# Kernel tuning notes

Hardware: AMD Instinct MI355X
Metric: run time of the kernel (lower is better)

## Reference

```python
import jax, jax.numpy as jnp
import numpy as np

BATCH = 2      # batch_size (number of videos)
NUM_HEADS = 8


def setup_inputs() -> dict:
    key = jax.random.key(0)
    k1, k2, k3 = jax.random.split(key, 3)
    B, H, W, C = 16, 64, 64, 512
    return {
        "hidden_states": jax.random.normal(k1, (B, H, W, C), dtype=jnp.float32),
        "w_qkv": jax.random.normal(k2, (3 * C, C), dtype=jnp.float32) * (C ** -0.5),
        "b_qkv": jax.random.normal(k3, (3 * C,), dtype=jnp.float32) * 0.02,
    }


def reference(hidden_states, w_qkv, b_qkv):
    B, H, W, C = hidden_states.shape
    bs, nh = BATCH, NUM_HEADS
    f = B // bs                      # video_length
    hd = C // nh                     # head_dim
    scale = hd ** -0.5

    # qkv projection (torch Linear: x @ W.T + b)
    qkv = hidden_states @ w_qkv.T + b_qkv                       # [B,H,W,3C]
    qkv = qkv.reshape(B, H * W, 3, nh, hd)
    qkv = qkv.transpose(2, 0, 3, 1, 4).reshape(3, B * nh, H * W, hd)
    q, k, v = qkv[0], qkv[1], qkv[2]                            # [B*nh, HW, hd]

    # NOTE: original rearrange labels '(b n f)' but memory layout is (b f) n;
    # it is a pure reshape, so replicate as flat reshape (faithful to math).
    q = q.reshape(bs, nh, f, H, W, hd)
    k = k.reshape(bs, nh, f, H, W, hd)
    v = v.reshape(bs, nh, f, H, W, hd)

    # q cat is identity; k/v: prepend last frame == cyclic roll by +1 on frames
    k = jnp.roll(k, 1, axis=2)
    v = jnp.roll(v, 1, axis=2)

    q = q.reshape(bs, nh, f, H * W, hd)
    # faithful flat reshape (scrambles (h,w,c) -> (hd, HW) order, as in torch)
    k = k.reshape(bs, nh, f, hd, H * W)
    v = v.reshape(bs, nh, f, H * W, hd)

    # einsums with NO contracted index: elementwise-transpose products
    attn = jnp.einsum('bnfhw,bnfwh->bnhfw', q * scale, k)       # [bs,nh,HW,f,hd]
    attn = jax.nn.softmax(attn, axis=-1)
    x = jnp.einsum('bnhfw,bnfhw->bnhfw', attn, v)               # [bs,nh,HW,f,hd]

    # faithful flat reshape (torch .view on contiguous tensor)
    x = x.reshape(bs, nh, f, H, W, hd)
    # rearrange 'b n f h w c -> (b f) h w (n c)'
    x = x.transpose(0, 2, 3, 4, 1, 5).reshape(bs * f, H, W, nh * hd)
    return x
```

## Files before the change

### kernel.cpp

```cpp
#include <hip/hip_runtime.h>
#include <math.h>


typedef _Float16 half8 __attribute__((ext_vector_type(8)));
typedef _Float16 half4 __attribute__((ext_vector_type(4)));
typedef __fp16 fp16x2 __attribute__((ext_vector_type(2)));
typedef float f32x4 __attribute__((ext_vector_type(4)));

__device__ __forceinline__ half8 pk8(const float4 x, const float4 y) {
    fp16x2 a = __builtin_amdgcn_cvt_pkrtz(x.x, x.y);
    fp16x2 b = __builtin_amdgcn_cvt_pkrtz(x.z, x.w);
    fp16x2 c = __builtin_amdgcn_cvt_pkrtz(y.x, y.y);
    fp16x2 d = __builtin_amdgcn_cvt_pkrtz(y.z, y.w);
    half8 r;
    r[0] = (_Float16)a[0]; r[1] = (_Float16)a[1];
    r[2] = (_Float16)b[0]; r[3] = (_Float16)b[1];
    r[4] = (_Float16)c[0]; r[5] = (_Float16)c[1];
    r[6] = (_Float16)d[0]; r[7] = (_Float16)d[1];
    return r;
}

__device__ __forceinline__ void gload_lds16(const void* g, void* l) {
    __builtin_amdgcn_global_load_lds(
        (const __attribute__((address_space(1))) unsigned int*)g,
        (__attribute__((address_space(3))) unsigned int*)l, 16, 0, 0);
}

__global__ __launch_bounds__(256) void cvt_fp16(
    const float* __restrict__ src, _Float16* __restrict__ dst)
{
    const size_t i = (size_t)blockIdx.x * 256 + threadIdx.x;
    const float4 x = *reinterpret_cast<const float4*>(src + i * 8);
    const float4 y = *reinterpret_cast<const float4*>(src + i * 8 + 4);
    *reinterpret_cast<half8*>(dst + i * 8) = pk8(x, y);
}

__global__ __launch_bounds__(256) void cvt_w_frag(
    const float* __restrict__ W, _Float16* __restrict__ Wf)
{
    const int gid  = blockIdx.x * 256 + threadIdx.x;
    const int lane = gid & 63;
    const int nf   = (gid >> 6) & 3;
    const int ks   = (gid >> 8) & 15;
    const int ntw  = gid >> 12;
    const float* src =
        W + (size_t)(ntw * 64 + nf * 16 + (lane & 15)) * 512 +
        ks * 32 + (lane >> 4) * 8;
    const float4 x = *reinterpret_cast<const float4*>(src);
    const float4 y = *reinterpret_cast<const float4*>(src + 4);
    *reinterpret_cast<half8*>(Wf + (size_t)gid * 8) = pk8(x, y);
}

__global__ __launch_bounds__(256, 4) void gemm_qkv_wf(
    const _Float16* __restrict__ Ah, const _Float16* __restrict__ Wf,
    const float* __restrict__ bias, _Float16* __restrict__ C)
{
    __shared__ __align__(16) _Float16 lds[12288];

    const int lin = blockIdx.x;
    const int swz = (lin & 7) * 768 + (lin >> 3);
    const int nt = swz % 12, mt = swz / 12;
    const int row0 = mt * 128, col0 = nt * 128;

    const int tid = threadIdx.x, wid = tid >> 6, lane = tid & 63;
    const int wm = wid >> 1, wn = wid & 1, l15 = lane & 15, kq = lane >> 4;

    const int s0  = wid * 2;
    const int rA0 = s0 * 16 + (lane >> 2);
    const int rA1 = rA0 + 16;
    const int c0  = (lane & 3) ^ ((rA0 >> 1) & 3);
    const int c1  = (lane & 3) ^ ((rA1 >> 1) & 3);
    const _Float16* ga0 = Ah + (size_t)(row0 + rA0) * 512 + c0 * 8;
    const _Float16* ga1 = Ah + (size_t)(row0 + rA1) * 512 + c1 * 8;

    const _Float16* wfb = Wf + (size_t)(nt * 2 + wn) * 32768 + lane * 8;

    f32x4 acc[4][4];
#pragma unroll
    for (int i = 0; i < 4; ++i)
#pragma unroll
        for (int j = 0; j < 4; ++j) acc[i][j] = (f32x4)0.f;

    half8 wfa[4], wfb_[4];

#define STAGE_A(KB, BUF)                                                       \
    do {                                                                       \
        _Float16* bdst = lds + (BUF) * 4096;                                   \
        gload_lds16(ga0 + (KB), bdst + s0 * 512);                              \
        gload_lds16(ga1 + (KB), bdst + (s0 + 1) * 512);                        \
    } while (0)

#define LOAD_W(DST, KS)                                                        \
    do {                                                                       \
        _Pragma("unroll")                                                      \
        for (int nf = 0; nf < 4; ++nf)                                         \
            DST[nf] = *reinterpret_cast<const half8*>(                         \
                wfb + (KS) * 2048 + nf * 512);                                 \
    } while (0)

#define FRAG_MFMA(BC, WU)                                                      \
    do {                                                                       \
        half8 ah[4];                                                           \
        _Pragma("unroll")                                                      \
        for (int mf = 0; mf < 4; ++mf) {                                       \
            const int r  = wm * 64 + mf * 16 + l15;                            \
            const int ph = (kq ^ ((r >> 1) & 3)) * 8;                          \
            ah[mf] = *reinterpret_cast<const half8*>((BC) + r * 32 + ph);      \
        }                                                                      \
        _Pragma("unroll")                                                      \
        for (int nf = 0; nf < 4; ++nf)                                         \
            _Pragma("unroll")                                                  \
            for (int mf = 0; mf < 4; ++mf)                                     \
                acc[mf][nf] = __builtin_amdgcn_mfma_f32_16x16x32_f16(          \
                    ah[mf], WU[nf], acc[mf][nf], 0, 0, 0);                     \
    } while (0)

#define STEP(T, WU, WL)                                                        \
    do {                                                                       \
        const int t2 = ((T) + 2 < 16) ? (T) + 2 : 15;                          \
        const int t1 = ((T) + 1 < 16) ? (T) + 1 : 15;                          \
        int sb = cb + 2; if (sb >= 3) sb -= 3;                                 \
        STAGE_A(t2 * 32, sb);                                                  \
        __builtin_amdgcn_sched_barrier(0);     \
        LOAD_W(WL, t1);                                                        \
        FRAG_MFMA(lds + cb * 4096, WU);                                        \
        __builtin_amdgcn_sched_barrier(0);                                     \
        __builtin_amdgcn_s_barrier();                                          \
        __builtin_amdgcn_sched_barrier(0);                                     \
        cb = (cb == 2) ? 0 : cb + 1;                                           \
    } while (0)

    STAGE_A(0, 0);
    STAGE_A(32, 1);
    __builtin_amdgcn_sched_barrier(0);
    LOAD_W(wfa, 0);
    asm volatile("s_waitcnt vmcnt(4)" ::: "memory");
    __builtin_amdgcn_sched_barrier(0);
    __builtin_amdgcn_s_barrier();
    __builtin_amdgcn_sched_barrier(0);

    int cb = 0;
#pragma unroll 1
    for (int t = 0; t < 16; t += 2) {
        STEP(t,     wfa, wfb_);
        STEP(t + 1, wfb_, wfa);
    }
#undef STEP
#undef FRAG_MFMA
#undef LOAD_W
#undef STAGE_A

    float* wbase = reinterpret_cast<float*>(lds) + wid * 1088;
    const float4 bv4 = *reinterpret_cast<const float4*>(
        &bias[col0 + wn * 64 + l15 * 4]);

#pragma unroll
    for (int mf = 0; mf < 4; ++mf) {
#pragma unroll
        for (int nf = 0; nf < 4; ++nf)
#pragma unroll
            for (int j = 0; j < 4; ++j)
                wbase[(kq * 4 + j) * 68 + nf * 16 + l15] = acc[mf][nf][j];
        __syncthreads();
#pragma unroll
        for (int i = 0; i < 4; ++i) {
            const int r16 = i * 4 + kq;
            float4 v = *reinterpret_cast<float4*>(wbase + r16 * 68 + l15 * 4);
            half4 h;
            h[0] = (_Float16)(v.x + bv4.x);
            h[1] = (_Float16)(v.y + bv4.y);
            h[2] = (_Float16)(v.z + bv4.z);
            h[3] = (_Float16)(v.w + bv4.w);
            const int r = row0 + wm * 64 + mf * 16 + r16;
            *reinterpret_cast<half4*>(
                &C[(size_t)r * 1536 + col0 + wn * 64 + l15 * 4]) = h;
        }
        __syncthreads();
    }
}

__global__ __launch_bounds__(256) void attn_scramble(
    const _Float16* __restrict__ qkv, float* __restrict__ out)
{
    __shared__ float Ks[64][68];
    const int bid = blockIdx.x;
    const int hw6 = bid & 63;
    const int n   = (bid >> 6) & 7;
    const int b   = bid >> 9;
    const int kn  = (n + 7) & 7;
    const int t   = threadIdx.x;
    {
        const int lx = t & 7;
        const int rp = t >> 3;
#pragma unroll
        for (int p = 0; p < 2; ++p) {
            const int dp = p * 32 + rp;
            const half8 kv = *reinterpret_cast<const half8*>(
                &qkv[(size_t)(b * 4096 + dp * 64 + hw6) * 1536 + 512 +
                     kn * 64 + lx * 8]);
#pragma unroll
            for (int e = 0; e < 8; ++e)
                Ks[lx * 8 + e][dp] = (float)kv[e];
        }
    }
    __syncthreads();
    const int row = t >> 2;
    const int tl  = t & 3;
    const size_t rbase = (size_t)(b * 4096 + hw6 * 64 + row) * 1536;
    float s[16];
    {
        const _Float16* qp = qkv + rbase + n * 64 + tl * 16;
        const half8 q0 = *reinterpret_cast<const half8*>(qp);
        const half8 q1 = *reinterpret_cast<const half8*>(qp + 8);
        float q[16], kk[16];
#pragma unroll
        for (int e = 0; e < 8; ++e) {
            q[e] = (float)q0[e];
            q[8 + e] = (float)q1[e];
        }
#pragma unroll
        for (int u = 0; u < 4; ++u)
            *reinterpret_cast<float4*>(&kk[u * 4]) =
                *reinterpret_cast<const float4*>(&Ks[row][tl * 16 + u * 4]);
        float m = -1e30f;
#pragma unroll
        for (int u = 0; u < 16; ++u) {
            s[u] = 0.125f * q[u] * kk[u];
            m = fmaxf(m, s[u]);
        }
        m = fmaxf(m, __shfl_xor(m, 1));
        m = fmaxf(m, __shfl_xor(m, 2));
        float sum = 0.f;
#pragma unroll
        for (int u = 0; u < 16; ++u) {
            s[u] = __expf(s[u] - m);
            sum += s[u];
        }
        sum += __shfl_xor(sum, 1);
        sum += __shfl_xor(sum, 2);
        const float inv = 1.0f / sum;
#pragma unroll
        for (int u = 0; u < 16; ++u) s[u] *= inv;
    }
    const _Float16* vp = qkv + rbase + 1024 + kn * 64 + tl * 16;
    const half8 v0 = *reinterpret_cast<const half8*>(vp);
    const half8 v1 = *reinterpret_cast<const half8*>(vp + 8);
    const int vb = b >> 3, fr = b & 7;
    float* op = out +
        ((size_t)(((vb * 8 + (hw6 >> 3)) * 64 + ((hw6 & 7) * 8 + (row >> 3))) * 64 +
                  ((row & 7) * 8 + n)) * 512) + fr * 64 + tl * 16;
    float4 o0, o1, o2, o3;
    o0.x = s[0]  * (float)v0[0]; o0.y = s[1]  * (float)v0[1];
    o0.z = s[2]  * (float)v0[2]; o0.w = s[3]  * (float)v0[3];
    o1.x = s[4]  * (float)v0[4]; o1.y = s[5]  * (float)v0[5];
    o1.z = s[6]  * (float)v0[6]; o1.w = s[7]  * (float)v0[7];
    o2.x = s[8]  * (float)v1[0]; o2.y = s[9]  * (float)v1[1];
    o2.z = s[10] * (float)v1[2]; o2.w = s[11] * (float)v1[3];
    o3.x = s[12] * (float)v1[4]; o3.y = s[13] * (float)v1[5];
    o3.z = s[14] * (float)v1[6]; o3.w = s[15] * (float)v1[7];
    *reinterpret_cast<float4*>(op)      = o0;
    *reinterpret_cast<float4*>(op + 4)  = o1;
    *reinterpret_cast<float4*>(op + 8)  = o2;
    *reinterpret_cast<float4*>(op + 12) = o3;
}

extern "C" void kernel_launch(void* const* d_in, const int* in_sizes, int n_in,
                              void* d_out, int out_size, void* d_ws, size_t ws_size,
                              hipStream_t stream) {
    const float* hs = (const float*)d_in[0];
    const float* w  = (const float*)d_in[1];
    const float* bq = (const float*)d_in[2];
    float* out = (float*)d_out;
    _Float16* qkv = (_Float16*)d_ws;

    _Float16* Asp = (_Float16*)d_out;
    _Float16* Wf  = Asp + 33554432;

    cvt_fp16<<<16384, 256, 0, stream>>>(hs, Asp);
    cvt_w_frag<<<384, 256, 0, stream>>>(w, Wf);
    gemm_qkv_wf<<<6144, 256, 0, stream>>>(Asp, Wf, bq, qkv);
    attn_scramble<<<8192, 256, 0, stream>>>(qkv, out);
}
```

Measured before the change: 234.7 us.

## Fuse fp32-to-fp16 activation conversion into QKV GEMM A-tile staging

Drops the separate cvt_fp16 pass over hidden_states. The GEMM now streams fp32 A tiles into LDS with direct global-to-LDS loads and converts them to fp16 fragments just before the MFMAs. This removes a full read and write of the 64M-element activation, but it doubles the A bytes per tile in LDS and in global traffic inside the GEMM. The LDS footprint grows to 48KB, so the occupancy hint drops from 4 to 3 blocks per CU, and the wait count and swizzle change to match.

```diff
diff --git a/kernel.cpp b/kernel.cpp
--- a/kernel.cpp
+++ b/kernel.cpp
@@ -24,15 +24,6 @@
     __builtin_amdgcn_global_load_lds(
         (const __attribute__((address_space(1))) unsigned int*)g,
         (__attribute__((address_space(3))) unsigned int*)l, 16, 0, 0);
-}
-
-__global__ __launch_bounds__(256) void cvt_fp16(
-    const float* __restrict__ src, _Float16* __restrict__ dst)
-{
-    const size_t i = (size_t)blockIdx.x * 256 + threadIdx.x;
-    const float4 x = *reinterpret_cast<const float4*>(src + i * 8);
-    const float4 y = *reinterpret_cast<const float4*>(src + i * 8 + 4);
-    *reinterpret_cast<half8*>(dst + i * 8) = pk8(x, y);
 }
 
 __global__ __launch_bounds__(256) void cvt_w_frag(
@@ -51,11 +42,11 @@
     *reinterpret_cast<half8*>(Wf + (size_t)gid * 8) = pk8(x, y);
 }
 
-__global__ __launch_bounds__(256, 4) void gemm_qkv_wf(
-    const _Float16* __restrict__ Ah, const _Float16* __restrict__ Wf,
+__global__ __launch_bounds__(256, 3) void gemm_qkv_a32(
+    const float* __restrict__ A, const _Float16* __restrict__ Wf,
     const float* __restrict__ bias, _Float16* __restrict__ C)
 {
-    __shared__ __align__(16) _Float16 lds[12288];
+    __shared__ __align__(16) float ldsf[12288];
 
     const int lin = blockIdx.x;
     const int swz = (lin & 7) * 768 + (lin >> 3);
@@ -65,13 +56,14 @@
     const int tid = threadIdx.x, wid = tid >> 6, lane = tid & 63;
     const int wm = wid >> 1, wn = wid & 1, l15 = lane & 15, kq = lane >> 4;
 
-    const int s0  = wid * 2;
-    const int rA0 = s0 * 16 + (lane >> 2);
-    const int rA1 = rA0 + 16;
-    const int c0  = (lane & 3) ^ ((rA0 >> 1) & 3);
-    const int c1  = (lane & 3) ^ ((rA1 >> 1) & 3);
-    const _Float16* ga0 = Ah + (size_t)(row0 + rA0) * 512 + c0 * 8;
-    const _Float16* ga1 = Ah + (size_t)(row0 + rA1) * 512 + c1 * 8;
+    const int s0 = wid * 4;
+    const int cA = (lane & 7) ^ (lane >> 3);
+    const float* ga[4];
+#pragma unroll
+    for (int i = 0; i < 4; ++i) {
+        const int rA = (s0 + i) * 8 + (lane >> 3);
+        ga[i] = A + (size_t)(row0 + rA) * 512 + cA * 4;
+    }
 
     const _Float16* wfb = Wf + (size_t)(nt * 2 + wn) * 32768 + lane * 8;
 
@@ -85,9 +77,11 @@
 
 #define STAGE_A(KB, BUF)                                                       \
     do {                                                                       \
-        _Float16* bdst = lds + (BUF) * 4096;                                   \
-        gload_lds16(ga0 + (KB), bdst + s0 * 512);                              \
-        gload_lds16(ga1 + (KB), bdst + (s0 + 1) * 512);                        \
+        float* bdst = ldsf + (BUF) * 4096;                                     \
+        gload_lds16(ga[0] + (KB), bdst + (s0 + 0) * 256);                      \
+        gload_lds16(ga[1] + (KB), bdst + (s0 + 1) * 256);                      \
+        gload_lds16(ga[2] + (KB), bdst + (s0 + 2) * 256);                      \
+        gload_lds16(ga[3] + (KB), bdst + (s0 + 3) * 256);                      \
     } while (0)
 
 #define LOAD_W(DST, KS)                                                        \
@@ -103,9 +97,14 @@
         half8 ah[4];                                                           \
         _Pragma("unroll")                                                      \
         for (int mf = 0; mf < 4; ++mf) {                                       \
-            const int r  = wm * 64 + mf * 16 + l15;                            \
-            const int ph = (kq ^ ((r >> 1) & 3)) * 8;                          \
-            ah[mf] = *reinterpret_cast<const half8*>((BC) + r * 32 + ph);      \
+            const int r   = wm * 64 + mf * 16 + l15;                           \
+            const int ph0 = ((2 * kq + 0) ^ (r & 7)) * 4;                      \
+            const int ph1 = ((2 * kq + 1) ^ (r & 7)) * 4;                      \
+            const float4 a0 = *reinterpret_cast<const float4*>(                \
+                (BC) + r * 32 + ph0);                                          \
+            const float4 a1 = *reinterpret_cast<const float4*>(                \
+                (BC) + r * 32 + ph1);                                          \
+            ah[mf] = pk8(a0, a1);                                              \
         }                                                                      \
         _Pragma("unroll")                                                      \
         for (int nf = 0; nf < 4; ++nf)                                         \
@@ -123,7 +122,7 @@
         STAGE_A(t2 * 32, sb);                                                  \
         __builtin_amdgcn_sched_barrier(0);     \
         LOAD_W(WL, t1);                                                        \
-        FRAG_MFMA(lds + cb * 4096, WU);                                        \
+        FRAG_MFMA(ldsf + cb * 4096, WU);                                       \
         __builtin_amdgcn_sched_barrier(0);                                     \
         __builtin_amdgcn_s_barrier();                                          \
         __builtin_amdgcn_sched_barrier(0);                                     \
@@ -134,7 +133,7 @@
     STAGE_A(32, 1);
     __builtin_amdgcn_sched_barrier(0);
     LOAD_W(wfa, 0);
-    asm volatile("s_waitcnt vmcnt(4)" ::: "memory");
+    asm volatile("s_waitcnt vmcnt(8)" ::: "memory");
     __builtin_amdgcn_sched_barrier(0);
     __builtin_amdgcn_s_barrier();
     __builtin_amdgcn_sched_barrier(0);
@@ -150,7 +149,7 @@
 #undef LOAD_W
 #undef STAGE_A
 
-    float* wbase = reinterpret_cast<float*>(lds) + wid * 1088;
+    float* wbase = ldsf + wid * 1088;
     const float4 bv4 = *reinterpret_cast<const float4*>(
         &bias[col0 + wn * 64 + l15 * 4]);
 
@@ -273,11 +272,9 @@
     float* out = (float*)d_out;
     _Float16* qkv = (_Float16*)d_ws;
 
-    _Float16* Asp = (_Float16*)d_out;
-    _Float16* Wf  = Asp + 33554432;
-
-    cvt_fp16<<<16384, 256, 0, stream>>>(hs, Asp);
+    _Float16* Wf = (_Float16*)d_out;
+
     cvt_w_frag<<<384, 256, 0, stream>>>(w, Wf);
-    gemm_qkv_wf<<<6144, 256, 0, stream>>>(Asp, Wf, bq, qkv);
+    gemm_qkv_a32<<<6144, 256, 0, stream>>>(hs, Wf, bq, qkv);
     attn_scramble<<<8192, 256, 0, stream>>>(qkv, out);
 }
```

New measurement: 286.5 us. 1.22x slower.
